# Kernel tuning notes

Hardware: AMD Instinct MI355X
Metric: run time of the kernel (lower is better)

Reference implementation:

```python
import jax, jax.numpy as jnp
import numpy as np
from jax import lax

EPS = 1e-4


def setup_inputs() -> dict:
    key = jax.random.key(0)
    k1, k2, k3, k4, k5 = jax.random.split(key, 5)
    B, F, P, C = 8192, 512, 64, 100
    return {
        "x": jax.random.normal(k1, (B, F), dtype=jnp.float32),
        "w": jax.random.normal(k2, (P, F), dtype=jnp.float32),
        "xi": jax.random.normal(k3, (1, P), dtype=jnp.float32),
        "eta": jax.random.normal(k4, (1, P), dtype=jnp.float32),
        "beta": jax.random.normal(k5, (P, C), dtype=jnp.float32),
    }


def reference(x, w, xi, eta, beta):
    # Distance layer: squared Euclidean distance to each prototype -> [B, P]
    # ||w_p - x||^2 expressed as GEMM form (same math, efficient)
    d = (jnp.sum(x * x, axis=-1, keepdims=True)
         - 2.0 * (x @ w.T)
         + jnp.sum(w * w, axis=-1))  # [B, P]

    # Distance activation: si = sigmoid(xi) * exp(-eta^2 * d), scaled by per-sample max
    gamma = eta * eta                       # [1, P]
    alpha = jax.nn.sigmoid(xi)              # [1, P]
    si = jnp.exp(-gamma * d) * alpha        # [B, P]
    si = si / (jnp.max(si, axis=-1, keepdims=True) + EPS)

    # Belief masses: u_p normalized beta^2 rows -> mass [B, P, C]
    beta_sq = beta * beta
    u = beta_sq / jnp.sum(beta_sq, axis=-1, keepdims=True)  # [P, C]
    mass = si[..., None] * u[None]                           # [B, P, C]

    # Omega: append residual uncertainty channel -> [B, P, C+1]
    omega = 1.0 - jnp.sum(mass, axis=-1, keepdims=True)
    mass_omega = jnp.concatenate([mass, omega], axis=-1)

    # Sequential Dempster combination over prototypes
    masses = jnp.moveaxis(mass_omega, 1, 0)  # [P, B, C+1]

    def step(m1, m2):
        omega1 = m1[..., -1:]
        omega2 = m2[..., -1:]
        c = m1 * m2 + m1 * omega2 + omega1 * m2
        c = c / (jnp.sum(c, axis=-1, keepdims=True) + EPS)
        return c, None

    m_final, _ = lax.scan(step, masses[0], masses[1:])  # [B, C+1]

    # Final normalization
    return m_final / jnp.sum(m_final, axis=-1, keepdims=True)
```

## Files before the change

kernel.cpp:

```cpp
#include <hip/hip_runtime.h>
#include <math.h>

#define NB 8192
#define NF 512
#define NP 64
#define NC 100
#define EPSF 1e-4f
#define LOG2E 1.44269504088896340736f

#define DPRE_OFF   0ull
#define DPRE_SZ    (4ull*NB*NP*4ull)
#define XSQP_OFF   (DPRE_OFF + DPRE_SZ)
#define XSQP_SZ    (4ull*NB*4ull)
#define UPAD_OFF   (XSQP_OFF + XSQP_SZ)
#define UPAD_SZ    (NP*128ull*4ull)
#define WSQ_OFF    (UPAD_OFF + UPAD_SZ)
#define KGAM_OFF   (WSQ_OFF + 256ull)
#define ALPH_OFF   (KGAM_OFF + 256ull)

__global__ __launch_bounds__(256)
void ds_k1(const float* __restrict__ x, const float* __restrict__ w,
           const float* __restrict__ xi, const float* __restrict__ eta,
           const float* __restrict__ beta,
           float* __restrict__ dpre, float* __restrict__ xsqp,
           float* __restrict__ upad, float* __restrict__ wsq,
           float* __restrict__ kgam, float* __restrict__ alph)
{
  const int blk = blockIdx.x;
  const int t   = threadIdx.x;

  if (blk == 512) {
    if (t < NP) {
      const int p = t;
      float s2 = 0.f;
      for (int k = 0; k < NF; k += 4) {
        float4 v = *(const float4*)&w[(size_t)p*NF + k];
        s2 += v.x*v.x + v.y*v.y + v.z*v.z + v.w*v.w;
      }
      wsq[p] = s2;
      float e = eta[p];
      kgam[p] = -LOG2E * e * e;
      alph[p] = 1.f / (1.f + __expf(-xi[p]));
      float bs = 0.f;
      for (int c = 0; c < NC; ++c) { float b = beta[p*NC + c]; bs += b*b; }
      float inv = 1.f / bs;
      for (int c = 0; c < NC; ++c) { float b = beta[p*NC + c]; upad[p*128 + c] = b*b*inv; }
      for (int c = NC; c < 128; ++c) upad[p*128 + c] = 0.f;
    }
    return;
  }

  __shared__ __align__(16) float xt[64][36];
  __shared__ float wt[64][33];
  __shared__ float sqp[64][17];
  const int s     = blk & 3;
  const int R0    = (blk >> 2) * 64;
  const int kbase = s * 128;
  const int r0 = (t >> 4) * 4;
  const int p0 = (t & 15) * 4;
  float acc[4][4] = {{0.f}};
  float xacc = 0.f;

  for (int cch = 0; cch < 2; ++cch) {
    const int kc = kbase + 64 * cch;
    __syncthreads();
    #pragma unroll
    for (int u = 0; u < 4; ++u) {
      const int idx = t + 256 * u;
      const int row = idx >> 4;
      const int kf  = (idx & 15) * 4;
      float4 v = *(const float4*)&x[(size_t)(R0 + row) * NF + kc + kf];
      sqp[row][idx & 15] = v.x*v.x + v.y*v.y + v.z*v.z + v.w*v.w;
      *(float4*)&xt[row][kf] = v;
      float4 wv = *(const float4*)&w[(size_t)row * NF + kc + kf];
      wt[row][kf]   = wv.x; wt[row][kf+1] = wv.y;
      wt[row][kf+2] = wv.z; wt[row][kf+3] = wv.w;
    }
    __syncthreads();
    if (t < 64) {
      #pragma unroll
      for (int q = 0; q < 16; ++q) xacc += sqp[t][q];
    }
    #pragma unroll 8
    for (int kk = 0; kk < 64; ++kk) {
      float a0 = xt[r0+0][kk], a1 = xt[r0+1][kk], a2 = xt[r0+2][kk], a3 = xt[r0+3][kk];
      float b0 = wt[p0+0][kk], b1 = wt[p0+1][kk], b2 = wt[p0+2][kk], b3 = wt[p0+3][kk];
      acc[0][0] = fmaf(a0,b0,acc[0][0]); acc[0][1] = fmaf(a0,b1,acc[0][1]);
      acc[0][2] = fmaf(a0,b2,acc[0][2]); acc[0][3] = fmaf(a0,b3,acc[0][3]);
      acc[1][0] = fmaf(a1,b0,acc[1][0]); acc[1][1] = fmaf(a1,b1,acc[1][1]);
      acc[1][2] = fmaf(a1,b2,acc[1][2]); acc[1][3] = fmaf(a1,b3,acc[1][3]);
      acc[2][0] = fmaf(a2,b0,acc[2][0]); acc[2][1] = fmaf(a2,b1,acc[2][1]);
      acc[2][2] = fmaf(a2,b2,acc[2][2]); acc[2][3] = fmaf(a2,b3,acc[2][3]);
      acc[3][0] = fmaf(a3,b0,acc[3][0]); acc[3][1] = fmaf(a3,b1,acc[3][1]);
      acc[3][2] = fmaf(a3,b2,acc[3][2]); acc[3][3] = fmaf(a3,b3,acc[3][3]);
    }
  }
  #pragma unroll
  for (int i = 0; i < 4; ++i) {
    float4 st = make_float4(acc[i][0], acc[i][1], acc[i][2], acc[i][3]);
    *(float4*)&dpre[((size_t)s * NB + R0 + r0 + i) * NP + p0] = st;
  }
  if (t < 64) xsqp[(size_t)s * NB + R0 + t] = xacc;
}

__global__ __launch_bounds__(256)
void ds_k2(const float* __restrict__ dpre, const float* __restrict__ xsqp,
           const float* __restrict__ upad, const float* __restrict__ wsq,
           const float* __restrict__ kgam, const float* __restrict__ alph,
           float* __restrict__ out)
{
  __shared__ __align__(16) float u_lds[NP * 128];
  __shared__ float si_lds[8][64];
  const int t = threadIdx.x;

  #pragma unroll
  for (int uu = 0; uu < 8; ++uu) {
    const int idx = (t + 256 * uu) * 4;
    *(float4*)&u_lds[idx] = *(const float4*)&upad[idx];
  }

  const int r    = t >> 5;
  const int lane = t & 31;
  const int grow = blockIdx.x * 8 + r;
  const int p2   = lane * 2;

  float dot0 = 0.f, dot1 = 0.f, xs = 0.f;
  #pragma unroll
  for (int s = 0; s < 4; ++s) {
    float2 v = *(const float2*)&dpre[((size_t)s * NB + grow) * NP + p2];
    dot0 += v.x; dot1 += v.y;
    xs   += xsqp[(size_t)s * NB + grow];
  }
  float d0  = xs + wsq[p2]   - 2.f * dot0;
  float d1  = xs + wsq[p2+1] - 2.f * dot1;
  float si0 = alph[p2]   * exp2f(kgam[p2]   * d0);
  float si1 = alph[p2+1] * exp2f(kgam[p2+1] * d1);
  float mx  = fmaxf(si0, si1);
  #pragma unroll
  for (int msk = 1; msk < 32; msk <<= 1) mx = fmaxf(mx, __shfl_xor(mx, msk, 64));
  float rinv = 1.f / (mx + EPSF);
  *(float2*)&si_lds[r][p2] = make_float2(si0 * rinv, si1 * rinv);
  __syncthreads();

  const bool isom = (lane == 25);
  float4 u0 = *(const float4*)&u_lds[lane * 4];
  float sp  = si_lds[r][0];
  float m0 = sp * u0.x, m1 = sp * u0.y, m2 = sp * u0.z, m3 = sp * u0.w;
  float om1 = 1.f - sp;
  if (isom) m0 = om1;

  for (int p = 1; p < NP; ++p) {
    sp = si_lds[r][p];
    float4 u = *(const float4*)&u_lds[p * 128 + lane * 4];
    float om2 = 1.f - sp;
    float nom = -(om1 * om2);
    float t20 = fmaf(sp, u.x, om2);
    t20 = isom ? (om2 + om2) : t20;
    float t21 = fmaf(sp, u.y, om2);
    float t22 = fmaf(sp, u.z, om2);
    float t23 = fmaf(sp, u.w, om2);
    m0 = fmaf(m0 + om1, t20, nom);
    m1 = fmaf(m1 + om1, t21, nom);
    m2 = fmaf(m2 + om1, t22, nom);
    m3 = fmaf(m3 + om1, t23, nom);
    om1 = fmaf(nom, -2.f, -nom);
    if (isom) m0 = om1;
    if ((p & 3) == 0) {
      float ss = (m0 + m1) + (m2 + m3);
      #pragma unroll
      for (int msk = 1; msk < 32; msk <<= 1) ss += __shfl_xor(ss, msk, 64);
      float rn = __builtin_amdgcn_rcpf(ss);
      m0 *= rn; m1 *= rn; m2 *= rn; m3 *= rn; om1 *= rn;
    }
  }

  float ss = (m0 + m1) + (m2 + m3);
  #pragma unroll
  for (int msk = 1; msk < 32; msk <<= 1) ss += __shfl_xor(ss, msk, 64);
  float rn = 1.f / ss;
  m0 *= rn; m1 *= rn; m2 *= rn; m3 *= rn;

  float* orow = &out[(size_t)grow * 101];
  if (lane < 25) {
    orow[lane*4+0] = m0; orow[lane*4+1] = m1;
    orow[lane*4+2] = m2; orow[lane*4+3] = m3;
  } else if (lane == 25) {
    orow[100] = m0;
  }
}

extern "C" void kernel_launch(void* const* d_in, const int* in_sizes, int n_in,
                              void* d_out, int out_size, void* d_ws, size_t ws_size,
                              hipStream_t stream)
{
  const float* x    = (const float*)d_in[0];
  const float* w    = (const float*)d_in[1];
  const float* xi   = (const float*)d_in[2];
  const float* eta  = (const float*)d_in[3];
  const float* beta = (const float*)d_in[4];
  char* ws = (char*)d_ws;
  float* dpre = (float*)(ws + DPRE_OFF);
  float* xsqp = (float*)(ws + XSQP_OFF);
  float* upad = (float*)(ws + UPAD_OFF);
  float* wsqp = (float*)(ws + WSQ_OFF);
  float* kgam = (float*)(ws + KGAM_OFF);
  float* alph = (float*)(ws + ALPH_OFF);

  hipLaunchKernelGGL(ds_k1, dim3(513), dim3(256), 0, stream,
                     x, w, xi, eta, beta, dpre, xsqp, upad, wsqp, kgam, alph);
  hipLaunchKernelGGL(ds_k2, dim3(1024), dim3(256), 0, stream,
                     dpre, xsqp, upad, wsqp, kgam, alph, (float*)d_out);
}
```

Before: 101.1 us.

## Fuse distance GEMM, parameter prep and Dempster scan into one kernel

Replaces the split-K GEMM kernel and the combination kernel with a single kernel. Each 8-row block computes its own dot products against w staged through LDS, plus the squared norms, sigmoid/gamma and normalized beta masses, then runs the Dempster scan. This removes the workspace round trip for partial dot products and one kernel launch. The cost is redundant per-block recomputation of w norms and u, and every block rereading all of w.

```diff
diff --git a/kernel.cpp b/kernel.cpp
--- a/kernel.cpp
+++ b/kernel.cpp
@@ -8,150 +8,155 @@
 #define EPSF 1e-4f
 #define LOG2E 1.44269504088896340736f
 
-#define DPRE_OFF   0ull
-#define DPRE_SZ    (4ull*NB*NP*4ull)
-#define XSQP_OFF   (DPRE_OFF + DPRE_SZ)
-#define XSQP_SZ    (4ull*NB*4ull)
-#define UPAD_OFF   (XSQP_OFF + XSQP_SZ)
-#define UPAD_SZ    (NP*128ull*4ull)
-#define WSQ_OFF    (UPAD_OFF + UPAD_SZ)
-#define KGAM_OFF   (WSQ_OFF + 256ull)
-#define ALPH_OFF   (KGAM_OFF + 256ull)
-
-__global__ __launch_bounds__(256)
-void ds_k1(const float* __restrict__ x, const float* __restrict__ w,
-           const float* __restrict__ xi, const float* __restrict__ eta,
-           const float* __restrict__ beta,
-           float* __restrict__ dpre, float* __restrict__ xsqp,
-           float* __restrict__ upad, float* __restrict__ wsq,
-           float* __restrict__ kgam, float* __restrict__ alph)
+__global__ __launch_bounds__(256, 4)
+void ds_fused(const float* __restrict__ x, const float* __restrict__ w,
+              const float* __restrict__ xi, const float* __restrict__ eta,
+              const float* __restrict__ beta, float* __restrict__ out)
 {
-  const int blk = blockIdx.x;
-  const int t   = threadIdx.x;
-
-  if (blk == 512) {
-    if (t < NP) {
-      const int p = t;
-      float s2 = 0.f;
-      for (int k = 0; k < NF; k += 4) {
-        float4 v = *(const float4*)&w[(size_t)p*NF + k];
-        s2 += v.x*v.x + v.y*v.y + v.z*v.z + v.w*v.w;
+  __shared__ __align__(16) float uni[64 * 132];
+  __shared__ __align__(16) float si_lds[8 * 64];
+  __shared__ float wqp[256];
+  __shared__ float wsql[64];
+  __shared__ float xsql[8];
+  float* wchT = uni;
+  float* upad = uni;
+
+  const int t  = threadIdx.x;
+  const int h  = t & 31;
+  const int rg = t >> 5;
+  const int R0 = blockIdx.x * 8;
+  const float* xrow = x + (size_t)(R0 + rg) * NF;
+
+  float dot0 = 0.f, dot1 = 0.f;
+  float4 wpf[4];
+  #pragma unroll
+  for (int j = 0; j < 4; ++j) {
+    const int f = t + 256 * j;
+    const int p = f >> 4, kq = f & 15;
+    wpf[j] = *(const float4*)&w[(size_t)p * NF + kq * 4];
+  }
+  for (int ch = 0; ch < 8; ++ch) {
+    const int kc = ch * 64;
+    __syncthreads();
+    #pragma unroll
+    for (int j = 0; j < 4; ++j) {
+      const int f = t + 256 * j;
+      const int p = f >> 4, kq = f & 15;
+      wchT[(kq*4+0)*66 + p] = wpf[j].x;
+      wchT[(kq*4+1)*66 + p] = wpf[j].y;
+      wchT[(kq*4+2)*66 + p] = wpf[j].z;
+      wchT[(kq*4+3)*66 + p] = wpf[j].w;
+    }
+    __syncthreads();
+    if (ch < 7) {
+      #pragma unroll
+      for (int j = 0; j < 4; ++j) {
+        const int f = t + 256 * j;
+        const int p = f >> 4, kq = f & 15;
+        wpf[j] = *(const float4*)&w[(size_t)p * NF + (kc + 64) + kq * 4];
       }
-      wsq[p] = s2;
-      float e = eta[p];
-      kgam[p] = -LOG2E * e * e;
-      alph[p] = 1.f / (1.f + __expf(-xi[p]));
-      float bs = 0.f;
-      for (int c = 0; c < NC; ++c) { float b = beta[p*NC + c]; bs += b*b; }
-      float inv = 1.f / bs;
-      for (int c = 0; c < NC; ++c) { float b = beta[p*NC + c]; upad[p*128 + c] = b*b*inv; }
-      for (int c = NC; c < 128; ++c) upad[p*128 + c] = 0.f;
-    }
-    return;
-  }
-
-  __shared__ __align__(16) float xt[64][36];
-  __shared__ float wt[64][33];
-  __shared__ float sqp[64][17];
-  const int s     = blk & 3;
-  const int R0    = (blk >> 2) * 64;
-  const int kbase = s * 128;
-  const int r0 = (t >> 4) * 4;
-  const int p0 = (t & 15) * 4;
-  float acc[4][4] = {{0.f}};
-  float xacc = 0.f;
-
-  for (int cch = 0; cch < 2; ++cch) {
-    const int kc = kbase + 64 * cch;
-    __syncthreads();
-    #pragma unroll
-    for (int u = 0; u < 4; ++u) {
-      const int idx = t + 256 * u;
-      const int row = idx >> 4;
-      const int kf  = (idx & 15) * 4;
-      float4 v = *(const float4*)&x[(size_t)(R0 + row) * NF + kc + kf];
-      sqp[row][idx & 15] = v.x*v.x + v.y*v.y + v.z*v.z + v.w*v.w;
-      *(float4*)&xt[row][kf] = v;
-      float4 wv = *(const float4*)&w[(size_t)row * NF + kc + kf];
-      wt[row][kf]   = wv.x; wt[row][kf+1] = wv.y;
-      wt[row][kf+2] = wv.z; wt[row][kf+3] = wv.w;
-    }
-    __syncthreads();
-    if (t < 64) {
-      #pragma unroll
-      for (int q = 0; q < 16; ++q) xacc += sqp[t][q];
-    }
+    }
+    #pragma unroll 4
+    for (int kq = 0; kq < 16; ++kq) {
+      float4 xv = *(const float4*)&xrow[kc + kq * 4];
+      float2 w0 = *(const float2*)&wchT[(kq*4+0)*66 + 2*h];
+      float2 w1 = *(const float2*)&wchT[(kq*4+1)*66 + 2*h];
+      float2 w2 = *(const float2*)&wchT[(kq*4+2)*66 + 2*h];
+      float2 w3 = *(const float2*)&wchT[(kq*4+3)*66 + 2*h];
+      dot0 = fmaf(xv.x, w0.x, dot0); dot1 = fmaf(xv.x, w0.y, dot1);
+      dot0 = fmaf(xv.y, w1.x, dot0); dot1 = fmaf(xv.y, w1.y, dot1);
+      dot0 = fmaf(xv.z, w2.x, dot0); dot1 = fmaf(xv.z, w2.y, dot1);
+      dot0 = fmaf(xv.w, w3.x, dot0); dot1 = fmaf(xv.w, w3.y, dot1);
+    }
+  }
+
+  {
+    const int rw = t >> 5, sl = t & 31;
+    const float* xr = x + (size_t)(R0 + rw) * NF + sl * 16;
+    float s = 0.f;
+    #pragma unroll
+    for (int j = 0; j < 4; ++j) {
+      float4 v = *(const float4*)&xr[j * 4];
+      s += v.x*v.x + v.y*v.y + v.z*v.z + v.w*v.w;
+    }
+    si_lds[t] = s;
+  }
+  {
+    const int p = t & 63, hf = t >> 6;
+    const float* wr = w + (size_t)p * NF + hf * 128;
+    float s = 0.f;
     #pragma unroll 8
-    for (int kk = 0; kk < 64; ++kk) {
-      float a0 = xt[r0+0][kk], a1 = xt[r0+1][kk], a2 = xt[r0+2][kk], a3 = xt[r0+3][kk];
-      float b0 = wt[p0+0][kk], b1 = wt[p0+1][kk], b2 = wt[p0+2][kk], b3 = wt[p0+3][kk];
-      acc[0][0] = fmaf(a0,b0,acc[0][0]); acc[0][1] = fmaf(a0,b1,acc[0][1]);
-      acc[0][2] = fmaf(a0,b2,acc[0][2]); acc[0][3] = fmaf(a0,b3,acc[0][3]);
-      acc[1][0] = fmaf(a1,b0,acc[1][0]); acc[1][1] = fmaf(a1,b1,acc[1][1]);
-      acc[1][2] = fmaf(a1,b2,acc[1][2]); acc[1][3] = fmaf(a1,b3,acc[1][3]);
-      acc[2][0] = fmaf(a2,b0,acc[2][0]); acc[2][1] = fmaf(a2,b1,acc[2][1]);
-      acc[2][2] = fmaf(a2,b2,acc[2][2]); acc[2][3] = fmaf(a2,b3,acc[2][3]);
-      acc[3][0] = fmaf(a3,b0,acc[3][0]); acc[3][1] = fmaf(a3,b1,acc[3][1]);
-      acc[3][2] = fmaf(a3,b2,acc[3][2]); acc[3][3] = fmaf(a3,b3,acc[3][3]);
-    }
-  }
-  #pragma unroll
-  for (int i = 0; i < 4; ++i) {
-    float4 st = make_float4(acc[i][0], acc[i][1], acc[i][2], acc[i][3]);
-    *(float4*)&dpre[((size_t)s * NB + R0 + r0 + i) * NP + p0] = st;
-  }
-  if (t < 64) xsqp[(size_t)s * NB + R0 + t] = xacc;
-}
-
-__global__ __launch_bounds__(256)
-void ds_k2(const float* __restrict__ dpre, const float* __restrict__ xsqp,
-           const float* __restrict__ upad, const float* __restrict__ wsq,
-           const float* __restrict__ kgam, const float* __restrict__ alph,
-           float* __restrict__ out)
-{
-  __shared__ __align__(16) float u_lds[NP * 128];
-  __shared__ float si_lds[8][64];
-  const int t = threadIdx.x;
-
-  #pragma unroll
-  for (int uu = 0; uu < 8; ++uu) {
-    const int idx = (t + 256 * uu) * 4;
-    *(float4*)&u_lds[idx] = *(const float4*)&upad[idx];
-  }
-
-  const int r    = t >> 5;
-  const int lane = t & 31;
-  const int grow = blockIdx.x * 8 + r;
-  const int p2   = lane * 2;
-
-  float dot0 = 0.f, dot1 = 0.f, xs = 0.f;
-  #pragma unroll
-  for (int s = 0; s < 4; ++s) {
-    float2 v = *(const float2*)&dpre[((size_t)s * NB + grow) * NP + p2];
-    dot0 += v.x; dot1 += v.y;
-    xs   += xsqp[(size_t)s * NB + grow];
-  }
-  float d0  = xs + wsq[p2]   - 2.f * dot0;
-  float d1  = xs + wsq[p2+1] - 2.f * dot1;
-  float si0 = alph[p2]   * exp2f(kgam[p2]   * d0);
-  float si1 = alph[p2+1] * exp2f(kgam[p2+1] * d1);
-  float mx  = fmaxf(si0, si1);
-  #pragma unroll
-  for (int msk = 1; msk < 32; msk <<= 1) mx = fmaxf(mx, __shfl_xor(mx, msk, 64));
-  float rinv = 1.f / (mx + EPSF);
-  *(float2*)&si_lds[r][p2] = make_float2(si0 * rinv, si1 * rinv);
-  __syncthreads();
-
-  const bool isom = (lane == 25);
-  float4 u0 = *(const float4*)&u_lds[lane * 4];
-  float sp  = si_lds[r][0];
+    for (int j = 0; j < 32; ++j) {
+      float4 v = *(const float4*)&wr[j * 4];
+      s += v.x*v.x + v.y*v.y + v.z*v.z + v.w*v.w;
+    }
+    wqp[hf * 64 + p] = s;
+  }
+  __syncthreads();
+  if (t < 8) {
+    float s = 0.f;
+    #pragma unroll
+    for (int i = 0; i < 32; ++i) s += si_lds[t * 32 + i];
+    xsql[t] = s;
+  }
+  if (t < 64) wsql[t] = ((wqp[t] + wqp[64 + t]) + wqp[128 + t]) + wqp[192 + t];
+  __syncthreads();
+
+  {
+    const float xs = xsql[rg];
+    const float d0 = xs + wsql[2*h]   - 2.f * dot0;
+    const float d1 = xs + wsql[2*h+1] - 2.f * dot1;
+    const float e0 = eta[2*h], e1 = eta[2*h+1];
+    const float g0 = -LOG2E * e0 * e0, g1 = -LOG2E * e1 * e1;
+    const float a0 = 1.f / (1.f + __expf(-xi[2*h]));
+    const float a1 = 1.f / (1.f + __expf(-xi[2*h+1]));
+    float si0 = a0 * exp2f(g0 * d0);
+    float si1 = a1 * exp2f(g1 * d1);
+    float mx = fmaxf(si0, si1);
+    #pragma unroll
+    for (int msk = 1; msk < 32; msk <<= 1) mx = fmaxf(mx, __shfl_xor(mx, msk, 64));
+    const float rinv = 1.f / (mx + EPSF);
+    *(float2*)&si_lds[rg * 64 + 2*h] = make_float2(si0 * rinv, si1 * rinv);
+  }
+
+  {
+    const int p4 = t >> 2, q4 = t & 3;
+    const float* br = beta + p4 * NC + q4 * 25;
+    float s = 0.f;
+    #pragma unroll 5
+    for (int j = 0; j < 25; ++j) { float b = br[j]; s = fmaf(b, b, s); }
+    wqp[q4 * 64 + p4] = s;
+  }
+  __syncthreads();
+  if (t < 64) wsql[t] = 1.f / (((wqp[t] + wqp[64 + t]) + wqp[128 + t]) + wqp[192 + t]);
+  __syncthreads();
+  {
+    const int p4 = t >> 2, q4 = t & 3;
+    const float bi = wsql[p4];
+    #pragma unroll
+    for (int i = 0; i < 8; ++i) {
+      const int q = q4 + 4 * i;
+      float4 uv = make_float4(0.f, 0.f, 0.f, 0.f);
+      if (q < 25) {
+        const float* br = beta + p4 * NC + q * 4;
+        float b0 = br[0], b1 = br[1], b2 = br[2], b3 = br[3];
+        uv = make_float4(b0*b0*bi, b1*b1*bi, b2*b2*bi, b3*b3*bi);
+      }
+      *(float4*)&upad[p4 * 132 + q * 4] = uv;
+    }
+  }
+  __syncthreads();
+
+  const bool isom = (h == 25);
+  float4 u0 = *(const float4*)&upad[h * 4];
+  float sp  = si_lds[rg * 64];
   float m0 = sp * u0.x, m1 = sp * u0.y, m2 = sp * u0.z, m3 = sp * u0.w;
   float om1 = 1.f - sp;
   if (isom) m0 = om1;
 
   for (int p = 1; p < NP; ++p) {
-    sp = si_lds[r][p];
-    float4 u = *(const float4*)&u_lds[p * 128 + lane * 4];
+    sp = si_lds[rg * 64 + p];
+    float4 u = *(const float4*)&upad[p * 132 + h * 4];
     float om2 = 1.f - sp;
     float nom = -(om1 * om2);
     float t20 = fmaf(sp, u.x, om2);
@@ -180,11 +185,11 @@
   float rn = 1.f / ss;
   m0 *= rn; m1 *= rn; m2 *= rn; m3 *= rn;
 
-  float* orow = &out[(size_t)grow * 101];
-  if (lane < 25) {
-    orow[lane*4+0] = m0; orow[lane*4+1] = m1;
-    orow[lane*4+2] = m2; orow[lane*4+3] = m3;
-  } else if (lane == 25) {
+  float* orow = &out[(size_t)(R0 + rg) * 101];
+  if (h < 25) {
+    orow[h*4+0] = m0; orow[h*4+1] = m1;
+    orow[h*4+2] = m2; orow[h*4+3] = m3;
+  } else if (h == 25) {
     orow[100] = m0;
   }
 }
@@ -198,16 +203,7 @@
   const float* xi   = (const float*)d_in[2];
   const float* eta  = (const float*)d_in[3];
   const float* beta = (const float*)d_in[4];
-  char* ws = (char*)d_ws;
-  float* dpre = (float*)(ws + DPRE_OFF);
-  float* xsqp = (float*)(ws + XSQP_OFF);
-  float* upad = (float*)(ws + UPAD_OFF);
-  float* wsqp = (float*)(ws + WSQ_OFF);
-  float* kgam = (float*)(ws + KGAM_OFF);
-  float* alph = (float*)(ws + ALPH_OFF);
-
-  hipLaunchKernelGGL(ds_k1, dim3(513), dim3(256), 0, stream,
-                     x, w, xi, eta, beta, dpre, xsqp, upad, wsqp, kgam, alph);
-  hipLaunchKernelGGL(ds_k2, dim3(1024), dim3(256), 0, stream,
-                     dpre, xsqp, upad, wsqp, kgam, alph, (float*)d_out);
+  (void)d_ws; (void)ws_size;
+  hipLaunchKernelGGL(ds_fused, dim3(1024), dim3(256), 0, stream,
+                     x, w, xi, eta, beta, (float*)d_out);
 }
```

New measurement: 119.9 us. +18.7%, slower.

## Split GEMM K into eight slices, transpose W tile, parallelize parameter prep

Applied to the files above, without the earlier changes.

The distance GEMM now splits K into 8 slices of 64 instead of 4 slices of 128, doubling the grid to 1024 GEMM blocks with one LDS load per block. W is stored transposed in LDS so the inner loop uses float4 LDS reads for both operands. The parameter-prep block spreads the w-norm and beta-normalisation work across all 256 threads instead of 64, and both kernels get occupancy hints in launch_bounds. The cost is twice as much partial-sum traffic through dpre/xsqp, which the second kernel must read back and reduce.

```diff
diff --git a/kernel.cpp b/kernel.cpp
--- a/kernel.cpp
+++ b/kernel.cpp
@@ -5,20 +5,21 @@
 #define NF 512
 #define NP 64
 #define NC 100
+#define NSP 8
 #define EPSF 1e-4f
 #define LOG2E 1.44269504088896340736f
 
 #define DPRE_OFF   0ull
-#define DPRE_SZ    (4ull*NB*NP*4ull)
+#define DPRE_SZ    ((size_t)NSP*NB*NP*4ull)
 #define XSQP_OFF   (DPRE_OFF + DPRE_SZ)
-#define XSQP_SZ    (4ull*NB*4ull)
+#define XSQP_SZ    ((size_t)NSP*NB*4ull)
 #define UPAD_OFF   (XSQP_OFF + XSQP_SZ)
 #define UPAD_SZ    (NP*128ull*4ull)
 #define WSQ_OFF    (UPAD_OFF + UPAD_SZ)
 #define KGAM_OFF   (WSQ_OFF + 256ull)
 #define ALPH_OFF   (KGAM_OFF + 256ull)
 
-__global__ __launch_bounds__(256)
+__global__ __launch_bounds__(256, 4)
 void ds_k1(const float* __restrict__ x, const float* __restrict__ w,
            const float* __restrict__ xi, const float* __restrict__ eta,
            const float* __restrict__ beta,
@@ -26,75 +27,114 @@
            float* __restrict__ upad, float* __restrict__ wsq,
            float* __restrict__ kgam, float* __restrict__ alph)
 {
+  __shared__ __align__(16) float xt[64][68];
+  __shared__ __align__(16) float wtT[64][68];
+  __shared__ float sqp[64][17];
   const int blk = blockIdx.x;
   const int t   = threadIdx.x;
 
-  if (blk == 512) {
-    if (t < NP) {
-      const int p = t;
-      float s2 = 0.f;
-      for (int k = 0; k < NF; k += 4) {
-        float4 v = *(const float4*)&w[(size_t)p*NF + k];
-        s2 += v.x*v.x + v.y*v.y + v.z*v.z + v.w*v.w;
+  if (blk == 1024) {
+    __shared__ float red[256];
+    {
+      const int p = t & 63, q = t >> 6;
+      const float* wr = w + (size_t)p * NF + q * 128;
+      float s = 0.f;
+      #pragma unroll 8
+      for (int j = 0; j < 32; ++j) {
+        float4 v = *(const float4*)&wr[j * 4];
+        s += v.x*v.x + v.y*v.y + v.z*v.z + v.w*v.w;
       }
-      wsq[p] = s2;
-      float e = eta[p];
-      kgam[p] = -LOG2E * e * e;
-      alph[p] = 1.f / (1.f + __expf(-xi[p]));
-      float bs = 0.f;
-      for (int c = 0; c < NC; ++c) { float b = beta[p*NC + c]; bs += b*b; }
-      float inv = 1.f / bs;
-      for (int c = 0; c < NC; ++c) { float b = beta[p*NC + c]; upad[p*128 + c] = b*b*inv; }
-      for (int c = NC; c < 128; ++c) upad[p*128 + c] = 0.f;
+      red[q * 64 + p] = s;
+    }
+    __syncthreads();
+    if (t < 64) {
+      wsq[t] = ((red[t] + red[64 + t]) + red[128 + t]) + red[192 + t];
+      float e = eta[t];
+      kgam[t] = -LOG2E * e * e;
+      alph[t] = 1.f / (1.f + __expf(-xi[t]));
+    }
+    __syncthreads();
+    {
+      const int p4 = t >> 2, q4 = t & 3;
+      const float* br = beta + p4 * NC + q4 * 25;
+      float s = 0.f;
+      #pragma unroll 5
+      for (int j = 0; j < 25; ++j) { float b = br[j]; s = fmaf(b, b, s); }
+      red[q4 * 64 + p4] = s;
+    }
+    __syncthreads();
+    __shared__ float binv[64];
+    if (t < 64) binv[t] = 1.f / (((red[t] + red[64 + t]) + red[128 + t]) + red[192 + t]);
+    __syncthreads();
+    {
+      const int p4 = t >> 2, q4 = t & 3;
+      const float bi = binv[p4];
+      #pragma unroll
+      for (int i = 0; i < 8; ++i) {
+        const int q = q4 + 4 * i;
+        float4 uv = make_float4(0.f, 0.f, 0.f, 0.f);
+        if (q < 25) {
+          const float* br = beta + p4 * NC + q * 4;
+          float b0 = br[0], b1 = br[1], b2 = br[2], b3 = br[3];
+          uv = make_float4(b0*b0*bi, b1*b1*bi, b2*b2*bi, b3*b3*bi);
+        }
+        *(float4*)&upad[p4 * 128 + q * 4] = uv;
+      }
     }
     return;
   }
 
-  __shared__ __align__(16) float xt[64][36];
-  __shared__ float wt[64][33];
-  __shared__ float sqp[64][17];
-  const int s     = blk & 3;
-  const int R0    = (blk >> 2) * 64;
-  const int kbase = s * 128;
+  const int s  = blk & 7;
+  const int R0 = (blk >> 3) * 64;
+  const int kb = s * 64;
+
+  #pragma unroll
+  for (int j = 0; j < 4; ++j) {
+    const int f   = t + 256 * j;
+    const int row = f >> 4;
+    const int kq  = f & 15;
+    float4 v = *(const float4*)&x[(size_t)(R0 + row) * NF + kb + kq * 4];
+    *(float4*)&xt[row][kq * 4] = v;
+    sqp[row][kq] = v.x*v.x + v.y*v.y + v.z*v.z + v.w*v.w;
+    float4 wv = *(const float4*)&w[(size_t)row * NF + kb + kq * 4];
+    wtT[kq*4+0][row] = wv.x; wtT[kq*4+1][row] = wv.y;
+    wtT[kq*4+2][row] = wv.z; wtT[kq*4+3][row] = wv.w;
+  }
+  __syncthreads();
+
+  float xacc = 0.f;
+  if (t < 64) {
+    #pragma unroll
+    for (int q = 0; q < 16; ++q) xacc += sqp[t][q];
+  }
+
   const int r0 = (t >> 4) * 4;
   const int p0 = (t & 15) * 4;
   float acc[4][4] = {{0.f}};
-  float xacc = 0.f;
-
-  for (int cch = 0; cch < 2; ++cch) {
-    const int kc = kbase + 64 * cch;
-    __syncthreads();
-    #pragma unroll
-    for (int u = 0; u < 4; ++u) {
-      const int idx = t + 256 * u;
-      const int row = idx >> 4;
-      const int kf  = (idx & 15) * 4;
-      float4 v = *(const float4*)&x[(size_t)(R0 + row) * NF + kc + kf];
-      sqp[row][idx & 15] = v.x*v.x + v.y*v.y + v.z*v.z + v.w*v.w;
-      *(float4*)&xt[row][kf] = v;
-      float4 wv = *(const float4*)&w[(size_t)row * NF + kc + kf];
-      wt[row][kf]   = wv.x; wt[row][kf+1] = wv.y;
-      wt[row][kf+2] = wv.z; wt[row][kf+3] = wv.w;
-    }
-    __syncthreads();
-    if (t < 64) {
-      #pragma unroll
-      for (int q = 0; q < 16; ++q) xacc += sqp[t][q];
-    }
-    #pragma unroll 8
-    for (int kk = 0; kk < 64; ++kk) {
-      float a0 = xt[r0+0][kk], a1 = xt[r0+1][kk], a2 = xt[r0+2][kk], a3 = xt[r0+3][kk];
-      float b0 = wt[p0+0][kk], b1 = wt[p0+1][kk], b2 = wt[p0+2][kk], b3 = wt[p0+3][kk];
-      acc[0][0] = fmaf(a0,b0,acc[0][0]); acc[0][1] = fmaf(a0,b1,acc[0][1]);
-      acc[0][2] = fmaf(a0,b2,acc[0][2]); acc[0][3] = fmaf(a0,b3,acc[0][3]);
-      acc[1][0] = fmaf(a1,b0,acc[1][0]); acc[1][1] = fmaf(a1,b1,acc[1][1]);
-      acc[1][2] = fmaf(a1,b2,acc[1][2]); acc[1][3] = fmaf(a1,b3,acc[1][3]);
-      acc[2][0] = fmaf(a2,b0,acc[2][0]); acc[2][1] = fmaf(a2,b1,acc[2][1]);
-      acc[2][2] = fmaf(a2,b2,acc[2][2]); acc[2][3] = fmaf(a2,b3,acc[2][3]);
-      acc[3][0] = fmaf(a3,b0,acc[3][0]); acc[3][1] = fmaf(a3,b1,acc[3][1]);
-      acc[3][2] = fmaf(a3,b2,acc[3][2]); acc[3][3] = fmaf(a3,b3,acc[3][3]);
-    }
-  }
+
+  #pragma unroll 4
+  for (int kq = 0; kq < 16; ++kq) {
+    float4 xv0 = *(const float4*)&xt[r0+0][kq*4];
+    float4 xv1 = *(const float4*)&xt[r0+1][kq*4];
+    float4 xv2 = *(const float4*)&xt[r0+2][kq*4];
+    float4 xv3 = *(const float4*)&xt[r0+3][kq*4];
+    float4 wv0 = *(const float4*)&wtT[kq*4+0][p0];
+    float4 wv1 = *(const float4*)&wtT[kq*4+1][p0];
+    float4 wv2 = *(const float4*)&wtT[kq*4+2][p0];
+    float4 wv3 = *(const float4*)&wtT[kq*4+3][p0];
+    #define ROWFMA(i, xv) \
+      acc[i][0] = fmaf(xv.x, wv0.x, acc[i][0]); acc[i][1] = fmaf(xv.x, wv0.y, acc[i][1]); \
+      acc[i][2] = fmaf(xv.x, wv0.z, acc[i][2]); acc[i][3] = fmaf(xv.x, wv0.w, acc[i][3]); \
+      acc[i][0] = fmaf(xv.y, wv1.x, acc[i][0]); acc[i][1] = fmaf(xv.y, wv1.y, acc[i][1]); \
+      acc[i][2] = fmaf(xv.y, wv1.z, acc[i][2]); acc[i][3] = fmaf(xv.y, wv1.w, acc[i][3]); \
+      acc[i][0] = fmaf(xv.z, wv2.x, acc[i][0]); acc[i][1] = fmaf(xv.z, wv2.y, acc[i][1]); \
+      acc[i][2] = fmaf(xv.z, wv2.z, acc[i][2]); acc[i][3] = fmaf(xv.z, wv2.w, acc[i][3]); \
+      acc[i][0] = fmaf(xv.w, wv3.x, acc[i][0]); acc[i][1] = fmaf(xv.w, wv3.y, acc[i][1]); \
+      acc[i][2] = fmaf(xv.w, wv3.z, acc[i][2]); acc[i][3] = fmaf(xv.w, wv3.w, acc[i][3]);
+    ROWFMA(0, xv0) ROWFMA(1, xv1) ROWFMA(2, xv2) ROWFMA(3, xv3)
+    #undef ROWFMA
+  }
+
   #pragma unroll
   for (int i = 0; i < 4; ++i) {
     float4 st = make_float4(acc[i][0], acc[i][1], acc[i][2], acc[i][3]);
@@ -103,7 +143,7 @@
   if (t < 64) xsqp[(size_t)s * NB + R0 + t] = xacc;
 }
 
-__global__ __launch_bounds__(256)
+__global__ __launch_bounds__(256, 4)
 void ds_k2(const float* __restrict__ dpre, const float* __restrict__ xsqp,
            const float* __restrict__ upad, const float* __restrict__ wsq,
            const float* __restrict__ kgam, const float* __restrict__ alph,
@@ -126,7 +166,7 @@
 
   float dot0 = 0.f, dot1 = 0.f, xs = 0.f;
   #pragma unroll
-  for (int s = 0; s < 4; ++s) {
+  for (int s = 0; s < NSP; ++s) {
     float2 v = *(const float2*)&dpre[((size_t)s * NB + grow) * NP + p2];
     dot0 += v.x; dot1 += v.y;
     xs   += xsqp[(size_t)s * NB + grow];
@@ -206,7 +246,7 @@
   float* kgam = (float*)(ws + KGAM_OFF);
   float* alph = (float*)(ws + ALPH_OFF);
 
-  hipLaunchKernelGGL(ds_k1, dim3(513), dim3(256), 0, stream,
+  hipLaunchKernelGGL(ds_k1, dim3(1025), dim3(256), 0, stream,
                      x, w, xi, eta, beta, dpre, xsqp, upad, wsqp, kgam, alph);
   hipLaunchKernelGGL(ds_k2, dim3(1024), dim3(256), 0, stream,
                      dpre, xsqp, upad, wsqp, kgam, alph, (float*)d_out);
```

Result: faster. 98.30 us (-2.7%).
